# Performance work log

Measured on AMD Instinct MI355X. Metric: run time of the kernel, lower is better.

## Reference

```python
import jax, jax.numpy as jnp
import numpy as np

NEG_SLOPE = 0.01  # torch LeakyReLU default

N_NODES = 100000
H_C = 128
N_EDGES = 1600000


def setup_inputs() -> dict:
    key = jax.random.key(0)
    k1, k2, k3, k4, k5, k6 = jax.random.split(key, 6)
    z = jax.random.normal(k1, (N_NODES, H_C), dtype=jnp.float32)
    edge_label_index = jax.random.randint(k2, (2, N_EDGES), 0, N_NODES, dtype=jnp.int64)
    # torch Linear: weight [out, in], bias [out]
    W1 = jax.random.normal(k3, (H_C, 2 * H_C), dtype=jnp.float32) / np.sqrt(2 * H_C)
    b1 = jax.random.normal(k4, (H_C,), dtype=jnp.float32) * 0.01
    W2 = jax.random.normal(k5, (1, H_C), dtype=jnp.float32) / np.sqrt(H_C)
    b2 = jax.random.normal(k6, (1,), dtype=jnp.float32) * 0.01
    return {"z": z, "edge_label_index": edge_label_index,
            "W1": W1, "b1": b1, "W2": W2, "b2": b2}


def reference(z, edge_label_index, W1, b1, W2, b2):
    row, col = edge_label_index[0], edge_label_index[1]
    # cat([z[row], z[col]], dim=1) @ W1.T == z[row] @ W1[:, :H].T + z[col] @ W1[:, H:].T
    h = z.shape[1]
    W1a, W1b = W1[:, :h], W1[:, h:]
    zc = jnp.einsum('eh,oh->eo', z[row], W1a) + jnp.einsum('eh,oh->eo', z[col], W1b) + b1
    zc = jnp.where(zc >= 0, zc, NEG_SLOPE * zc)  # LeakyReLU
    out = jnp.einsum('eh,oh->eo', zc, W2) + b2   # [E, 1]
    return out.reshape(-1)
```

## Files before the change

kernel.cpp:

```cpp
#include <hip/hip_runtime.h>
#include <hip/hip_fp16.h>

#define NN 100000
#define HC 128
#define NE 1600000

typedef float f32x4 __attribute__((ext_vector_type(4)));
typedef short bf16x8 __attribute__((ext_vector_type(8)));

__device__ __forceinline__ unsigned short f2bf(float f) {
  union { float f; unsigned u; } c; c.f = f;
  unsigned u = c.u + (0x7FFFu + ((c.u >> 16) & 1u));
  return (unsigned short)(u >> 16);
}
__device__ __forceinline__ float bf2f(unsigned short b) {
  union { unsigned u; float f; } c; c.u = ((unsigned)b) << 16;
  return c.f;
}

__global__ __launch_bounds__(256) void wprep_kernel(
    const float* __restrict__ W1, unsigned short* __restrict__ Wh,
    unsigned short* __restrict__ Wl) {
  const int idx = blockIdx.x * 256 + threadIdx.x;
  if (idx >= 256 * 128) return;
  const int o = idx >> 7;
  const int k = idx & 127;
  const float f = W1[(size_t)(o & 127) * 256 + ((o >> 7) << 7) + k];
  const unsigned short hi = f2bf(f);
  Wh[idx] = hi;
  Wl[idx] = f2bf(f - bf2f(hi));
}

__global__ __launch_bounds__(256) void precompute_uv_mfma4_kernel(
    const float* __restrict__ z, const unsigned short* __restrict__ Wh,
    const unsigned short* __restrict__ Wl, __half* __restrict__ UV) {
  const int lane = threadIdx.x & 63;
  const int wv = threadIdx.x >> 6;
  const int nb = blockIdx.x * 32;
  const int og = wv * 64;
  const int lr = lane & 15;
  const int lg = lane >> 4;

  bf16x8 bh[2][4], bl[2][4];
#pragma unroll
  for (int ms = 0; ms < 2; ++ms) {
    const int node = nb + ms * 16 + lr;
    const float* __restrict__ zp = z + (size_t)node * HC + lg * 8;
#pragma unroll
    for (int kg = 0; kg < 4; ++kg) {
      const float4 p0 = *(const float4*)(zp + kg * 32);
      const float4 p1 = *(const float4*)(zp + kg * 32 + 4);
      const float v[8] = {p0.x, p0.y, p0.z, p0.w, p1.x, p1.y, p1.z, p1.w};
#pragma unroll
      for (int e = 0; e < 8; ++e) {
        const unsigned short hi = f2bf(v[e]);
        bh[ms][kg][e] = (short)hi;
        bl[ms][kg][e] = (short)f2bf(v[e] - bf2f(hi));
      }
    }
  }

#pragma unroll 1
  for (int nt = 0; nt < 4; ++nt) {
    const int orow = og + nt * 16 + lr;
    const unsigned short* __restrict__ wph = Wh + orow * 128 + lg * 8;
    const unsigned short* __restrict__ wpl = Wl + orow * 128 + lg * 8;

    f32x4 acc0 = {0.f, 0.f, 0.f, 0.f};
    f32x4 acc1 = {0.f, 0.f, 0.f, 0.f};
#pragma unroll
    for (int kg = 0; kg < 4; ++kg) {
      const bf16x8 ah = *(const bf16x8*)(wph + kg * 32);
      const bf16x8 al = *(const bf16x8*)(wpl + kg * 32);
      acc0 = __builtin_amdgcn_mfma_f32_16x16x32_bf16(ah, bh[0][kg], acc0, 0, 0, 0);
      acc0 = __builtin_amdgcn_mfma_f32_16x16x32_bf16(al, bh[0][kg], acc0, 0, 0, 0);
      acc0 = __builtin_amdgcn_mfma_f32_16x16x32_bf16(ah, bl[0][kg], acc0, 0, 0, 0);
      acc1 = __builtin_amdgcn_mfma_f32_16x16x32_bf16(ah, bh[1][kg], acc1, 0, 0, 0);
      acc1 = __builtin_amdgcn_mfma_f32_16x16x32_bf16(al, bh[1][kg], acc1, 0, 0, 0);
      acc1 = __builtin_amdgcn_mfma_f32_16x16x32_bf16(ah, bl[1][kg], acc1, 0, 0, 0);
    }

    const int ob = og + nt * 16 + lg * 4;
    {
      const int node = nb + lr;
      union { uint2 u; __half2 h[2]; } pk;
      pk.h[0] = __floats2half2_rn(acc0[0], acc0[1]);
      pk.h[1] = __floats2half2_rn(acc0[2], acc0[3]);
      *(uint2*)(UV + (size_t)node * 256 + ob) = pk.u;
    }
    {
      const int node = nb + 16 + lr;
      union { uint2 u; __half2 h[2]; } pk;
      pk.h[0] = __floats2half2_rn(acc1[0], acc1[1]);
      pk.h[1] = __floats2half2_rn(acc1[2], acc1[3]);
      *(uint2*)(UV + (size_t)node * 256 + ob) = pk.u;
    }
  }
}

__global__ __launch_bounds__(256) void edge_decode_f16_kernel(
    const int* __restrict__ eidx, const __half* __restrict__ UV,
    const float* __restrict__ b1, const float* __restrict__ W2,
    const float* __restrict__ b2, float* __restrict__ out,
    int e0, int e1) {
  const int lane = threadIdx.x & 15;
  const int qw = (blockIdx.x * 256 + threadIdx.x) >> 4;
  const int nqw = (gridDim.x * 256) >> 4;

  const float4 b1a = ((const float4*)b1)[2 * lane];
  const float4 b1b = ((const float4*)b1)[2 * lane + 1];
  const float4 w2a = ((const float4*)W2)[2 * lane];
  const float4 w2b = ((const float4*)W2)[2 * lane + 1];
  const float bb[8] = {b1a.x, b1a.y, b1a.z, b1a.w, b1b.x, b1b.y, b1b.z, b1b.w};
  const float ww[8] = {w2a.x, w2a.y, w2a.z, w2a.w, w2b.x, w2b.y, w2b.z, w2b.w};
  const float bias2 = b2[0];

  const int* __restrict__ rows = eidx;
  const int* __restrict__ cols = eidx + NE;

#pragma unroll 2
  for (int e = e0 + qw; e < e1; e += nqw) {
    const int r = rows[e];
    const int c = cols[e];
    union { uint4 u; __half2 h[4]; } Uu, Vv;
    Uu.u = *(const uint4*)(UV + (size_t)r * 256 + lane * 8);
    Vv.u = *(const uint4*)(UV + (size_t)c * 256 + 128 + lane * 8);

    float s = 0.f;
#pragma unroll
    for (int k = 0; k < 4; ++k) {
      const float2 uf = __half22float2(Uu.h[k]);
      const float2 vf = __half22float2(Vv.h[k]);
      float t0 = uf.x + vf.x + bb[2 * k];
      t0 = (t0 >= 0.f) ? t0 : 0.01f * t0;
      s = fmaf(t0, ww[2 * k], s);
      float t1 = uf.y + vf.y + bb[2 * k + 1];
      t1 = (t1 >= 0.f) ? t1 : 0.01f * t1;
      s = fmaf(t1, ww[2 * k + 1], s);
    }

    s += __shfl_xor(s, 8);
    s += __shfl_xor(s, 4);
    s += __shfl_xor(s, 2);
    s += __shfl_xor(s, 1);
    if (lane == 0) out[e] = s + bias2;
  }
}

__global__ __launch_bounds__(64) void edge_direct_kernel(
    const float* __restrict__ z, const int* __restrict__ eidx,
    const float* __restrict__ W1, const float* __restrict__ b1,
    const float* __restrict__ W2, const float* __restrict__ b2,
    float* __restrict__ out) {
  const int lane = threadIdx.x;
  const int o0 = lane, o1 = lane + 64;
  const float w2_0 = W2[o0], w2_1 = W2[o1];
  const float b1_0 = b1[o0], b1_1 = b1[o1];
  const float bias2 = b2[0];

  for (int e = blockIdx.x; e < NE; e += gridDim.x) {
    const int r = eidx[e];
    const int c = eidx[e + NE];
    const float* __restrict__ zr = z + (size_t)r * HC;
    const float* __restrict__ zc = z + (size_t)c * HC;
    float a0 = 0.f, a1 = 0.f;
    for (int h = 0; h < HC; ++h) {
      const float zrh = zr[h], zch = zc[h];
      a0 = fmaf(zrh, W1[(size_t)o0 * 256 + h], a0);
      a0 = fmaf(zch, W1[(size_t)o0 * 256 + 128 + h], a0);
      a1 = fmaf(zrh, W1[(size_t)o1 * 256 + h], a1);
      a1 = fmaf(zch, W1[(size_t)o1 * 256 + 128 + h], a1);
    }
    a0 += b1_0; a1 += b1_1;
    a0 = (a0 >= 0.f) ? a0 : 0.01f * a0;
    a1 = (a1 >= 0.f) ? a1 : 0.01f * a1;
    float s = fmaf(a0, w2_0, a1 * w2_1);
    for (int off = 32; off >= 1; off >>= 1) s += __shfl_xor(s, off);
    if (lane == 0) out[e] = s + bias2;
  }
}

extern "C" void kernel_launch(void* const* d_in, const int* in_sizes, int n_in,
                              void* d_out, int out_size, void* d_ws, size_t ws_size,
                              hipStream_t stream) {
  const float* z  = (const float*)d_in[0];
  const int*   ei = (const int*)d_in[1];
  const float* W1 = (const float*)d_in[2];
  const float* b1 = (const float*)d_in[3];
  const float* W2 = (const float*)d_in[4];
  const float* b2 = (const float*)d_in[5];
  float* out = (float*)d_out;

  const size_t uv_bytes = (size_t)NN * 256 * sizeof(__half);
  const size_t w_bytes  = (size_t)256 * 128 * sizeof(unsigned short);

  if (ws_size >= uv_bytes + 2 * w_bytes) {
    __half* UV = (__half*)d_ws;
    unsigned short* Wh = (unsigned short*)((char*)d_ws + uv_bytes);
    unsigned short* Wl = Wh + 256 * 128;
    wprep_kernel<<<128, 256, 0, stream>>>(W1, Wh, Wl);
    precompute_uv_mfma4_kernel<<<NN / 32, 256, 0, stream>>>(z, Wh, Wl, UV);
    edge_decode_f16_kernel<<<2048, 256, 0, stream>>>(ei, UV, b1, W2, b2, out,
                                                     0, NE / 2);
    edge_decode_f16_kernel<<<2048, 256, 0, stream>>>(ei, UV, b1, W2, b2, out,
                                                     NE / 2, NE);
  } else {
    edge_direct_kernel<<<8192, 64, 0, stream>>>(z, ei, W1, b1, W2, b2, out);
  }
}
```

Measured before the change: 194.1 us.

## Stage z tiles through swizzled LDS and pre-pack W1 into MFMA fragment order

The node projection kernel now loads each block's 32x128 z tile with coalesced float4 reads into XOR-swizzled shared memory, then builds its bf16 hi/lo fragments from LDS instead of strided global reads. W1 is pre-packed into per-lane MFMA fragment order so each weight fragment load is a contiguous 16-byte read per lane. The edge decode is also split into four launches instead of two, likely for cache locality over edge ranges. This adds shared memory and a barrier per block, plus extra launch overhead.

```diff
diff --git a/kernel.cpp b/kernel.cpp
--- a/kernel.cpp
+++ b/kernel.cpp
@@ -18,38 +18,62 @@
   return c.f;
 }
 
-__global__ __launch_bounds__(256) void wprep_kernel(
-    const float* __restrict__ W1, unsigned short* __restrict__ Wh,
-    unsigned short* __restrict__ Wl) {
-  const int idx = blockIdx.x * 256 + threadIdx.x;
-  if (idx >= 256 * 128) return;
-  const int o = idx >> 7;
-  const int k = idx & 127;
-  const float f = W1[(size_t)(o & 127) * 256 + ((o >> 7) << 7) + k];
-  const unsigned short hi = f2bf(f);
-  Wh[idx] = hi;
-  Wl[idx] = f2bf(f - bf2f(hi));
-}
-
-__global__ __launch_bounds__(256) void precompute_uv_mfma4_kernel(
-    const float* __restrict__ z, const unsigned short* __restrict__ Wh,
-    const unsigned short* __restrict__ Wl, __half* __restrict__ UV) {
-  const int lane = threadIdx.x & 63;
-  const int wv = threadIdx.x >> 6;
-  const int nb = blockIdx.x * 32;
-  const int og = wv * 64;
+__global__ __launch_bounds__(256) void wprep2_kernel(
+    const float* __restrict__ W1, unsigned short* __restrict__ Whf,
+    unsigned short* __restrict__ Wlf) {
+  const int f = blockIdx.x * 256 + threadIdx.x;
+  if (f >= 4096) return;
+  const int lane = f & 63;
+  const int kg = (f >> 6) & 3;
+  const int ot = f >> 8;
   const int lr = lane & 15;
   const int lg = lane >> 4;
+  const int o = ot * 16 + lr;
+  const int kb = kg * 32 + lg * 8;
+  const float* __restrict__ src =
+      W1 + (size_t)(o & 127) * 256 + ((o >> 7) << 7) + kb;
+#pragma unroll
+  for (int e = 0; e < 8; ++e) {
+    const float v = src[e];
+    const unsigned short hi = f2bf(v);
+    Whf[(size_t)f * 8 + e] = hi;
+    Wlf[(size_t)f * 8 + e] = f2bf(v - bf2f(hi));
+  }
+}
+
+__global__ __launch_bounds__(256) void precompute_uv_mfma5_kernel(
+    const float* __restrict__ z, const unsigned short* __restrict__ Whf,
+    const unsigned short* __restrict__ Wlf, __half* __restrict__ UV) {
+  __shared__ char zs[32 * 512];
+
+  const int t = threadIdx.x;
+  const int lane = t & 63;
+  const int wv = t >> 6;
+  const int nb = blockIdx.x * 32;
+  const int lr = lane & 15;
+  const int lg = lane >> 4;
+
+#pragma unroll
+  for (int i = 0; i < 4; ++i) {
+    const int ci = t + 256 * i;
+    const int row = ci >> 5;
+    const int c16 = ci & 31;
+    const float4 v = *(const float4*)(z + (size_t)(nb + row) * HC + c16 * 4);
+    const int dst = (row * 512 + c16 * 16) ^ ((row & 7) << 4);
+    *(float4*)(zs + dst) = v;
+  }
+  __syncthreads();
 
   bf16x8 bh[2][4], bl[2][4];
 #pragma unroll
   for (int ms = 0; ms < 2; ++ms) {
-    const int node = nb + ms * 16 + lr;
-    const float* __restrict__ zp = z + (size_t)node * HC + lg * 8;
+    const int row = ms * 16 + lr;
+    const int sw = (row & 7) << 4;
 #pragma unroll
     for (int kg = 0; kg < 4; ++kg) {
-      const float4 p0 = *(const float4*)(zp + kg * 32);
-      const float4 p1 = *(const float4*)(zp + kg * 32 + 4);
+      const int c16 = kg * 8 + lg * 2;
+      const float4 p0 = *(const float4*)(zs + ((row * 512 + c16 * 16) ^ sw));
+      const float4 p1 = *(const float4*)(zs + ((row * 512 + (c16 + 1) * 16) ^ sw));
       const float v[8] = {p0.x, p0.y, p0.z, p0.w, p1.x, p1.y, p1.z, p1.w};
 #pragma unroll
       for (int e = 0; e < 8; ++e) {
@@ -62,16 +86,16 @@
 
 #pragma unroll 1
   for (int nt = 0; nt < 4; ++nt) {
-    const int orow = og + nt * 16 + lr;
-    const unsigned short* __restrict__ wph = Wh + orow * 128 + lg * 8;
-    const unsigned short* __restrict__ wpl = Wl + orow * 128 + lg * 8;
+    const int ot = wv * 4 + nt;
+    const unsigned short* __restrict__ wph = Whf + ((size_t)(ot * 4) * 64 + lane) * 8;
+    const unsigned short* __restrict__ wpl = Wlf + ((size_t)(ot * 4) * 64 + lane) * 8;
 
     f32x4 acc0 = {0.f, 0.f, 0.f, 0.f};
     f32x4 acc1 = {0.f, 0.f, 0.f, 0.f};
 #pragma unroll
     for (int kg = 0; kg < 4; ++kg) {
-      const bf16x8 ah = *(const bf16x8*)(wph + kg * 32);
-      const bf16x8 al = *(const bf16x8*)(wpl + kg * 32);
+      const bf16x8 ah = *(const bf16x8*)(wph + (size_t)kg * 64 * 8);
+      const bf16x8 al = *(const bf16x8*)(wpl + (size_t)kg * 64 * 8);
       acc0 = __builtin_amdgcn_mfma_f32_16x16x32_bf16(ah, bh[0][kg], acc0, 0, 0, 0);
       acc0 = __builtin_amdgcn_mfma_f32_16x16x32_bf16(al, bh[0][kg], acc0, 0, 0, 0);
       acc0 = __builtin_amdgcn_mfma_f32_16x16x32_bf16(ah, bl[0][kg], acc0, 0, 0, 0);
@@ -80,7 +104,7 @@
       acc1 = __builtin_amdgcn_mfma_f32_16x16x32_bf16(ah, bl[1][kg], acc1, 0, 0, 0);
     }
 
-    const int ob = og + nt * 16 + lg * 4;
+    const int ob = ot * 16 + lg * 4;
     {
       const int node = nb + lr;
       union { uint2 u; __half2 h[2]; } pk;
@@ -196,14 +220,14 @@
 
   if (ws_size >= uv_bytes + 2 * w_bytes) {
     __half* UV = (__half*)d_ws;
-    unsigned short* Wh = (unsigned short*)((char*)d_ws + uv_bytes);
-    unsigned short* Wl = Wh + 256 * 128;
-    wprep_kernel<<<128, 256, 0, stream>>>(W1, Wh, Wl);
-    precompute_uv_mfma4_kernel<<<NN / 32, 256, 0, stream>>>(z, Wh, Wl, UV);
-    edge_decode_f16_kernel<<<2048, 256, 0, stream>>>(ei, UV, b1, W2, b2, out,
-                                                     0, NE / 2);
-    edge_decode_f16_kernel<<<2048, 256, 0, stream>>>(ei, UV, b1, W2, b2, out,
-                                                     NE / 2, NE);
+    unsigned short* Whf = (unsigned short*)((char*)d_ws + uv_bytes);
+    unsigned short* Wlf = Whf + 256 * 128;
+    wprep2_kernel<<<16, 256, 0, stream>>>(W1, Whf, Wlf);
+    precompute_uv_mfma5_kernel<<<NN / 32, 256, 0, stream>>>(z, Whf, Wlf, UV);
+    for (int q = 0; q < 4; ++q) {
+      edge_decode_f16_kernel<<<2048, 256, 0, stream>>>(
+          ei, UV, b1, W2, b2, out, q * (NE / 4), (q + 1) * (NE / 4));
+    }
   } else {
     edge_direct_kernel<<<8192, 64, 0, stream>>>(z, ei, W1, b1, W2, b2, out);
   }
```

Measured after the change: 162.1 us. -16.5%, faster.
